# Performance work log

Measured on AMD Instinct MI355X. Metric: run time of the kernel, lower is better.

## Reference

```python
import jax, jax.numpy as jnp
import numpy as np

N_NODES = 50000
N_EDGES = 600000
BAG = 16
VOCAB = 10000
EMB = 128
HID = 128
N_CLASSES = 10
N_GRAPHS = 512
PAD_IDX = 1


def setup_inputs() -> dict:
    key = jax.random.key(0)
    ks = jax.random.split(key, 12)
    x_tokens = jax.random.randint(ks[0], (N_NODES, BAG), 0, VOCAB)
    src = jax.random.randint(ks[1], (N_EDGES,), 0, N_NODES)
    dst = jax.random.randint(ks[2], (N_EDGES,), 0, N_NODES)
    edge_index = jnp.stack([src, dst])
    batch = jnp.sort(jax.random.randint(ks[3], (N_NODES,), 0, N_GRAPHS))
    # rows 0,1 are zero in the original (weights[2:] filled from pretrained vectors)
    emb_table = (jax.random.normal(ks[4], (VOCAB, EMB)) * 0.02).at[:2].set(0.0)
    s = 1.0 / np.sqrt(EMB)
    w1_l = jax.random.normal(ks[5], (HID, EMB)) * s
    b1 = jnp.zeros((HID,), jnp.float32)
    w1_r = jax.random.normal(ks[6], (HID, EMB)) * s
    w2_l = jax.random.normal(ks[7], (HID, HID)) * s
    b2 = jnp.zeros((HID,), jnp.float32)
    w2_r = jax.random.normal(ks[8], (HID, HID)) * s
    w_out = jax.random.normal(ks[9], (N_CLASSES, HID)) * s
    b_out = jnp.zeros((N_CLASSES,), jnp.float32)
    return {"x_tokens": x_tokens, "edge_index": edge_index, "batch": batch,
            "emb_table": emb_table, "w1_l": w1_l, "b1": b1, "w1_r": w1_r,
            "w2_l": w2_l, "b2": b2, "w2_r": w2_r, "w_out": w_out, "b_out": b_out}


def _embedding_bag_mean(tokens, table):
    # nn.EmbeddingBag mode='mean' with padding_idx: padding tokens excluded from mean
    emb = table[tokens]                                  # [N, BAG, D]
    mask = (tokens != PAD_IDX)[..., None].astype(table.dtype)
    total = jnp.sum(emb * mask, axis=1)                  # [N, D]
    cnt = jnp.clip(jnp.sum(mask, axis=1), 1.0)           # [N, 1]
    return total / cnt


def _sage_conv(x, src, dst, w_l, b_l, w_r):
    # PyG SAGEConv: lin_l(mean_{j in N(i)} x_j) + lin_r(x_i); lin_r has no bias
    n = x.shape[0]
    msg_sum = jax.ops.segment_sum(x[src], dst, num_segments=n)           # [N, D]
    deg = jax.ops.segment_sum(jnp.ones((src.shape[0], 1), x.dtype), dst,
                              num_segments=n)                             # [N, 1]
    aggr = msg_sum / jnp.clip(deg, 1.0)
    return aggr @ w_l.T + b_l + x @ w_r.T


def reference(x_tokens, edge_index, batch, emb_table, w1_l, b1, w1_r,
              w2_l, b2, w2_r, w_out, b_out):
    src, dst = edge_index[0], edge_index[1]
    x = _embedding_bag_mean(x_tokens, emb_table)                 # [N, EMB]
    x = jax.nn.relu(_sage_conv(x, src, dst, w1_l, b1, w1_r))     # [N, HID]
    x = jax.nn.relu(_sage_conv(x, src, dst, w2_l, b2, w2_r))     # [N, HID]
    # global_mean_pool over graph ids
    g_sum = jax.ops.segment_sum(x, batch, num_segments=N_GRAPHS)
    g_cnt = jax.ops.segment_sum(jnp.ones((x.shape[0], 1), x.dtype), batch,
                                num_segments=N_GRAPHS)
    g = g_sum / jnp.clip(g_cnt, 1.0)                             # [G, HID]
    return g @ w_out.T + b_out                                   # [G, C]
```

## Files before the change

### kernel.cpp

```cpp
#include <hip/hip_runtime.h>
#include <hip/hip_bf16.h>

#define NN 50000
#define NE 600000
#define BAG 16
#define EMB 128
#define HID 128
#define NC 10
#define NG 512
#define PAD_IDX 1
#define VOCAB 10000
#define SLOTS 64
#define TPAIRS (VOCAB * EMB / 2)
#define WPAIRS (4 * HID * EMB / 2)
#define EMVB (NN / 16)
#define NCHUNK 293
#define SCB (NCHUNK * 8)
#define NRANGE (NN / 8)
#define NTILES ((NN + 127) / 128)

typedef __attribute__((ext_vector_type(8))) short v8s;
typedef __attribute__((ext_vector_type(4))) float v4f;

__device__ __forceinline__ float bflo(unsigned u) { return __uint_as_float(u << 16); }
__device__ __forceinline__ float bfhi(unsigned u) { return __uint_as_float(u & 0xffff0000u); }
__device__ __forceinline__ unsigned short f2bf(float f) {
    unsigned u = __float_as_uint(f);
    return (unsigned short)((u + 0x7fffu + ((u >> 16) & 1u)) >> 16);
}
__device__ __forceinline__ void acc8(float* a, v8s v) {
    unsigned* u = (unsigned*)&v;
#pragma unroll
    for (int j = 0; j < 4; j++) {
        a[2 * j] += bflo(u[j]);
        a[2 * j + 1] += bfhi(u[j]);
    }
}

__global__ void k_conv(const float* __restrict__ t, unsigned short* __restrict__ tb,
                       const float* __restrict__ w1l, const float* __restrict__ w1r,
                       const float* __restrict__ w2l, const float* __restrict__ w2r,
                       unsigned short* __restrict__ wbf, int* __restrict__ cnt,
                       float* __restrict__ gsum, float* __restrict__ gcnt) {
    int i = blockIdx.x * blockDim.x + threadIdx.x;
    if (i < NN) cnt[i] = 0;
    if (i < NG * HID) gsum[i] = 0.f;
    if (i < NG) gcnt[i] = 0.f;
    if (i < TPAIRS) {
        float2 v = *(const float2*)(t + (size_t)i * 2);
        unsigned lo = f2bf(v.x), hi = f2bf(v.y);
        *(unsigned*)(tb + (size_t)i * 2) = lo | (hi << 16);
    } else if (i < TPAIRS + WPAIRS) {
        int j = i - TPAIRS;
        int k = j * 2;
        int arr = k >> 14;
        int o = k & 16383;
        const float* w = (arr == 0) ? w1l : (arr == 1) ? w1r : (arr == 2) ? w2l : w2r;
        float2 v = *(const float2*)(w + o);
        unsigned lo = f2bf(v.x), hi = f2bf(v.y);
        *(unsigned*)(wbf + k) = lo | (hi << 16);
    }
}

__global__ __launch_bounds__(256) void k_scatem(const int* __restrict__ src,
                                                const int* __restrict__ dst,
                                                int* __restrict__ cnt,
                                                unsigned short* __restrict__ slots,
                                                const int* __restrict__ tokens,
                                                const unsigned short* __restrict__ table,
                                                unsigned short* __restrict__ x0) {
    int b = blockIdx.x;
    int tid = threadIdx.x;

    if (b < SCB) {
        int r = b & 7, c = b >> 3;
        int e0 = c * 2048 + tid * 8;
        if (e0 < NE) {
            int lo = r * NRANGE, hi = lo + NRANGE;
            int4 s0 = *((const int4*)(src + e0));
            int4 s1 = *((const int4*)(src + e0) + 1);
            int4 d0 = *((const int4*)(dst + e0));
            int4 d1 = *((const int4*)(dst + e0) + 1);
            int ss[8] = {s0.x, s0.y, s0.z, s0.w, s1.x, s1.y, s1.z, s1.w};
            int dd[8] = {d0.x, d0.y, d0.z, d0.w, d1.x, d1.y, d1.z, d1.w};
#pragma unroll
            for (int j = 0; j < 8; j++) {
                if (dd[j] >= lo && dd[j] < hi) {
                    int p = atomicAdd(&cnt[dd[j]], 1);
                    if (p < SLOTS)
                        slots[(size_t)dd[j] * SLOTS + p] = (unsigned short)ss[j];
                }
            }
        }
        return;
    }

    int sl = tid & 15;
    int node = (b - SCB) * 16 + (tid >> 4);
    const int* tp = tokens + node * BAG;
    int tk[16];
    *(int4*)(tk) = *(const int4*)(tp);
    *(int4*)(tk + 4) = *(const int4*)(tp + 4);
    *(int4*)(tk + 8) = *(const int4*)(tp + 8);
    *(int4*)(tk + 12) = *(const int4*)(tp + 12);
    int c = 0;
#pragma unroll
    for (int t = 0; t < BAG; t++) c += (tk[t] != PAD_IDX);
    float a[8];
#pragma unroll
    for (int j = 0; j < 8; j++) a[j] = 0.f;
#pragma unroll
    for (int h = 0; h < 2; h++) {
        v8s v[8];
#pragma unroll
        for (int t = 0; t < 8; t++)
            v[t] = *(const v8s*)(table + (size_t)tk[h * 8 + t] * EMB + sl * 8);
#pragma unroll
        for (int t = 0; t < 8; t++) acc8(a, v[t]);
    }
    float inv = 1.0f / (float)(c > 0 ? c : 1);
    uint4 o;
    o.x = f2bf(a[0] * inv) | ((unsigned)f2bf(a[1] * inv) << 16);
    o.y = f2bf(a[2] * inv) | ((unsigned)f2bf(a[3] * inv) << 16);
    o.z = f2bf(a[4] * inv) | ((unsigned)f2bf(a[5] * inv) << 16);
    o.w = f2bf(a[6] * inv) | ((unsigned)f2bf(a[7] * inv) << 16);
    *(uint4*)(x0 + (size_t)node * EMB + sl * 8) = o;
}

__global__ __launch_bounds__(256) void k_aggr(const unsigned short* __restrict__ x,
                                              const int* __restrict__ cnt,
                                              const unsigned short* __restrict__ slots,
                                              unsigned short* __restrict__ aggr) {
    int node = blockIdx.x * 4 + (threadIdx.x >> 6);
    int lane = threadIdx.x & 63;
    if (node >= NN) return;
    int deg = cnt[node];
    int m = deg > SLOTS ? SLOTS : deg;
    int g = lane >> 4, sl = lane & 15;
    float a[8];
#pragma unroll
    for (int j = 0; j < 8; j++) a[j] = 0.f;
    int idx_l = slots[(size_t)node * SLOTS + ((lane < m) ? lane : 0)];
    int i = 0;
    for (; i + 8 <= m; i += 8) {
        int t0 = __shfl(idx_l, i + g, 64);
        int t1 = __shfl(idx_l, i + 4 + g, 64);
        v8s v0 = *(const v8s*)(x + (size_t)t0 * HID + sl * 8);
        v8s v1 = *(const v8s*)(x + (size_t)t1 * HID + sl * 8);
        acc8(a, v0);
        acc8(a, v1);
    }
    for (; i + 4 <= m; i += 4) {
        int t0 = __shfl(idx_l, i + g, 64);
        v8s v0 = *(const v8s*)(x + (size_t)t0 * HID + sl * 8);
        acc8(a, v0);
    }
    int rem = m - i;
    if (rem > 0) {
        int t0 = __shfl(idx_l, (g < rem) ? i + g : i, 64);
        v8s v0 = *(const v8s*)(x + (size_t)t0 * HID + sl * 8);
        if (g < rem) acc8(a, v0);
    }
#pragma unroll
    for (int j = 0; j < 8; j++) {
        a[j] += __shfl_xor(a[j], 16, 64);
        a[j] += __shfl_xor(a[j], 32, 64);
    }
    float inv = 1.0f / (float)(deg > 0 ? deg : 1);
    if (g == 0) {
        uint4 o;
        o.x = f2bf(a[0] * inv) | ((unsigned)f2bf(a[1] * inv) << 16);
        o.y = f2bf(a[2] * inv) | ((unsigned)f2bf(a[3] * inv) << 16);
        o.z = f2bf(a[4] * inv) | ((unsigned)f2bf(a[5] * inv) << 16);
        o.w = f2bf(a[6] * inv) | ((unsigned)f2bf(a[7] * inv) << 16);
        *(uint4*)(aggr + (size_t)node * HID + sl * 8) = o;
    }
}

__device__ __forceinline__ void sage_kloop(int row0, const unsigned short* __restrict__ xa,
                                           const unsigned short* __restrict__ xr,
                                           const unsigned short* __restrict__ wl,
                                           const unsigned short* __restrict__ wr,
                                           unsigned short* As, unsigned short* Bs,
                                           v4f acc[2][8]) {
    int tid = threadIdx.x;
    int wave = tid >> 6, lane = tid & 63;
    int q = lane >> 4, l16 = lane & 15;
    for (int kc = 0; kc < 8; kc++) {
        const unsigned short* Ag = (kc < 4) ? xa : xr;
        const unsigned short* Bg = (kc < 4) ? wl : wr;
        int koff = (kc & 3) * 32;
#pragma unroll
        for (int it = 0; it < 2; it++) {
            int seg = tid + it * 256;
            int r = seg >> 2, sg = seg & 3;
            int gr = row0 + r;
            if (gr > NN - 1) gr = NN - 1;
            v8s a = *(const v8s*)(Ag + (size_t)gr * HID + koff + sg * 8);
            *(v8s*)(As + r * 32 + sg * 8) = a;
            v8s b = *(const v8s*)(Bg + (size_t)r * HID + koff + sg * 8);
            *(v8s*)(Bs + r * 32 + sg * 8) = b;
        }
        __syncthreads();
        v8s a0 = *(const v8s*)(As + (wave * 32 + l16) * 32 + q * 8);
        v8s a1 = *(const v8s*)(As + (wave * 32 + 16 + l16) * 32 + q * 8);
#pragma unroll
        for (int nt = 0; nt < 8; nt++) {
            v8s b = *(const v8s*)(Bs + (nt * 16 + l16) * 32 + q * 8);
            acc[0][nt] = __builtin_amdgcn_mfma_f32_16x16x32_bf16(a0, b, acc[0][nt], 0, 0, 0);
            acc[1][nt] = __builtin_amdgcn_mfma_f32_16x16x32_bf16(a1, b, acc[1][nt], 0, 0, 0);
        }
        __syncthreads();
    }
}

__global__ __launch_bounds__(256) void k_sage(const unsigned short* __restrict__ xa,
                                              const unsigned short* __restrict__ xr,
                                              const unsigned short* __restrict__ wl,
                                              const unsigned short* __restrict__ wr,
                                              const float* __restrict__ bias,
                                              unsigned short* __restrict__ out) {
    __shared__ unsigned short As[128 * 32];
    __shared__ unsigned short Bs[128 * 32];
    int row0 = blockIdx.x * 128;
    v4f acc[2][8];
#pragma unroll
    for (int m = 0; m < 2; m++)
#pragma unroll
        for (int n = 0; n < 8; n++) acc[m][n] = (v4f){0.f, 0.f, 0.f, 0.f};
    sage_kloop(row0, xa, xr, wl, wr, As, Bs, acc);
    int tid = threadIdx.x;
    int wave = tid >> 6, lane = tid & 63;
    int q = lane >> 4, l16 = lane & 15;
#pragma unroll
    for (int nt = 0; nt < 8; nt++) {
        int col = nt * 16 + l16;
        float bv = bias[col];
#pragma unroll
        for (int mt = 0; mt < 2; mt++) {
#pragma unroll
            for (int r = 0; r < 4; r++) {
                int row = row0 + wave * 32 + mt * 16 + q * 4 + r;
                if (row < NN) {
                    float v = acc[mt][nt][r] + bv;
                    v = v > 0.f ? v : 0.f;
                    out[(size_t)row * HID + col] = f2bf(v);
                }
            }
        }
    }
}

__global__ __launch_bounds__(256) void k_sagepool(const unsigned short* __restrict__ xa,
                                                  const unsigned short* __restrict__ xr,
                                                  const unsigned short* __restrict__ wl,
                                                  const unsigned short* __restrict__ wr,
                                                  const float* __restrict__ bias,
                                                  const int* __restrict__ batch,
                                                  float* __restrict__ gsum,
                                                  float* __restrict__ gcnt) {
    __shared__ unsigned short smem[128 * 128];
    unsigned short* As = smem;
    unsigned short* Bs = smem + 128 * 32;
    int row0 = blockIdx.x * 128;
    v4f acc[2][8];
#pragma unroll
    for (int m = 0; m < 2; m++)
#pragma unroll
        for (int n = 0; n < 8; n++) acc[m][n] = (v4f){0.f, 0.f, 0.f, 0.f};
    sage_kloop(row0, xa, xr, wl, wr, As, Bs, acc);
    int tid = threadIdx.x;
    int wave = tid >> 6, lane = tid & 63;
    int q = lane >> 4, l16 = lane & 15;
#pragma unroll
    for (int nt = 0; nt < 8; nt++) {
        int col = nt * 16 + l16;
        float bv = bias[col];
#pragma unroll
        for (int mt = 0; mt < 2; mt++) {
#pragma unroll
            for (int r = 0; r < 4; r++) {
                int rl = wave * 32 + mt * 16 + q * 4 + r;
                float v = acc[mt][nt][r] + bv;
                v = v > 0.f ? v : 0.f;
                smem[rl * 128 + col] = f2bf(v);
            }
        }
    }
    __syncthreads();
    if (tid < 128) {
        int col = tid;
        int end = NN - row0;
        if (end > 128) end = 128;
        int cur = batch[row0];
        float acc_p = 0.f;
        int c = 0;
        for (int i = 0; i < end; i++) {
            int b = batch[row0 + i];
            if (b != cur) {
                atomicAdd(&gsum[cur * HID + col], acc_p);
                if (col == 0) atomicAdd(&gcnt[cur], (float)c);
                acc_p = 0.f;
                c = 0;
                cur = b;
            }
            acc_p += __uint_as_float(((unsigned)smem[i * 128 + col]) << 16);
            c++;
        }
        atomicAdd(&gsum[cur * HID + col], acc_p);
        if (col == 0) atomicAdd(&gcnt[cur], (float)c);
    }
}

__global__ __launch_bounds__(128) void k_final(const float* __restrict__ gsum,
                                               const float* __restrict__ gcnt,
                                               const float* __restrict__ w_out,
                                               const float* __restrict__ b_out,
                                               float* __restrict__ out) {
    __shared__ float mean[HID];
    int g = blockIdx.x, tid = threadIdx.x;
    mean[tid] = gsum[g * HID + tid] / fmaxf(gcnt[g], 1.0f);
    __syncthreads();
    if (tid < NC) {
        float s = b_out[tid];
#pragma unroll 16
        for (int d = 0; d < HID; d++) s += mean[d] * w_out[tid * HID + d];
        out[g * NC + tid] = s;
    }
}

extern "C" void kernel_launch(void* const* d_in, const int* in_sizes, int n_in,
                              void* d_out, int out_size, void* d_ws, size_t ws_size,
                              hipStream_t stream) {
    const int* x_tokens = (const int*)d_in[0];
    const int* edge = (const int*)d_in[1];
    const int* batch = (const int*)d_in[2];
    const float* emb_table = (const float*)d_in[3];
    const float* w1l = (const float*)d_in[4];
    const float* b1 = (const float*)d_in[5];
    const float* w1r = (const float*)d_in[6];
    const float* w2l = (const float*)d_in[7];
    const float* b2 = (const float*)d_in[8];
    const float* w2r = (const float*)d_in[9];
    const float* w_out = (const float*)d_in[10];
    const float* b_out = (const float*)d_in[11];
    float* out = (float*)d_out;

    char* ws = (char*)d_ws;
    size_t off = 0;
    auto alloc = [&](size_t bytes) {
        void* p = ws + off;
        off += (bytes + 255) & ~(size_t)255;
        return p;
    };
    int* cnt = (int*)alloc(NN * 4);
    unsigned short* slots = (unsigned short*)alloc((size_t)NN * SLOTS * 2);
    unsigned short* wbf = (unsigned short*)alloc(4 * HID * EMB * 2);
    float* gsum = (float*)alloc(NG * HID * 4);
    float* gcnt = (float*)alloc(NG * 4);
    unsigned short* x0 = (unsigned short*)alloc((size_t)NN * EMB * 2);
    unsigned short* x1 = (unsigned short*)alloc((size_t)NN * HID * 2);
    unsigned short* aggrb = (unsigned short*)alloc((size_t)NN * HID * 2);
    unsigned short* table_bf = x1;

    const int* srcp = edge;
    const int* dstp = edge + NE;

    k_conv<<<(TPAIRS + WPAIRS + 255) / 256, 256, 0, stream>>>(
        emb_table, table_bf, w1l, w1r, w2l, w2r, wbf, cnt, gsum, gcnt);
    k_scatem<<<SCB + EMVB, 256, 0, stream>>>(srcp, dstp, cnt, slots, x_tokens,
                                             table_bf, x0);
    k_aggr<<<(NN + 3) / 4, 256, 0, stream>>>(x0, cnt, slots, aggrb);
    k_sage<<<NTILES, 256, 0, stream>>>(aggrb, x0, wbf, wbf + 16384, b1, x1);
    k_aggr<<<(NN + 3) / 4, 256, 0, stream>>>(x1, cnt, slots, aggrb);
    k_sagepool<<<NTILES, 256, 0, stream>>>(aggrb, x1, wbf + 32768, wbf + 49152, b2,
                                           batch, gsum, gcnt);
    k_final<<<NG, 128, 0, stream>>>(gsum, gcnt, w_out, b_out, out);
}
```

Measured before the change: 208.9 us.

## Build neighbor slots via LDS-binned queues and a per-range CSR kernel

Edge scattering no longer does one global atomic per edge into per-node counters. Each edge block first bins its edges by destination range (125 ranges of 400 nodes) in shared memory, then appends each bin to a per-range global queue with one atomic per bin. A new kernel builds each range's counts and slot lists in LDS and writes them out with coalesced stores. The aim is to cut global atomic traffic and scattered 2-byte writes. The cost is an extra launch, a queue buffer, and a large static LDS allocation in the fused scatter/embedding kernel, which may lower occupancy for the embedding blocks.

```diff
diff --git a/kernel.cpp b/kernel.cpp
--- a/kernel.cpp
+++ b/kernel.cpp
@@ -14,9 +14,10 @@
 #define TPAIRS (VOCAB * EMB / 2)
 #define WPAIRS (4 * HID * EMB / 2)
 #define EMVB (NN / 16)
-#define NCHUNK 293
-#define SCB (NCHUNK * 8)
-#define NRANGE (NN / 8)
+#define NCH1 293
+#define RANGES 125
+#define RNODES 400
+#define QCAP 6400
 #define NTILES ((NN + 127) / 128)
 
 typedef __attribute__((ext_vector_type(8))) short v8s;
@@ -40,10 +41,10 @@
 __global__ void k_conv(const float* __restrict__ t, unsigned short* __restrict__ tb,
                        const float* __restrict__ w1l, const float* __restrict__ w1r,
                        const float* __restrict__ w2l, const float* __restrict__ w2r,
-                       unsigned short* __restrict__ wbf, int* __restrict__ cnt,
+                       unsigned short* __restrict__ wbf, int* __restrict__ qtail,
                        float* __restrict__ gsum, float* __restrict__ gcnt) {
     int i = blockIdx.x * blockDim.x + threadIdx.x;
-    if (i < NN) cnt[i] = 0;
+    if (i < RANGES) qtail[i] = 0;
     if (i < NG * HID) gsum[i] = 0.f;
     if (i < NG) gcnt[i] = 0.f;
     if (i < TPAIRS) {
@@ -64,19 +65,21 @@
 
 __global__ __launch_bounds__(256) void k_scatem(const int* __restrict__ src,
                                                 const int* __restrict__ dst,
-                                                int* __restrict__ cnt,
-                                                unsigned short* __restrict__ slots,
+                                                int* __restrict__ qtail,
+                                                unsigned* __restrict__ queue,
                                                 const int* __restrict__ tokens,
                                                 const unsigned short* __restrict__ table,
                                                 unsigned short* __restrict__ x0) {
+    __shared__ int qcntL[RANGES];
+    __shared__ unsigned qbufL[RANGES * 64];
     int b = blockIdx.x;
     int tid = threadIdx.x;
 
-    if (b < SCB) {
-        int r = b & 7, c = b >> 3;
-        int e0 = c * 2048 + tid * 8;
+    if (b < NCH1) {
+        for (int i = tid; i < RANGES; i += 256) qcntL[i] = 0;
+        __syncthreads();
+        int e0 = b * 2048 + tid * 8;
         if (e0 < NE) {
-            int lo = r * NRANGE, hi = lo + NRANGE;
             int4 s0 = *((const int4*)(src + e0));
             int4 s1 = *((const int4*)(src + e0) + 1);
             int4 d0 = *((const int4*)(dst + e0));
@@ -85,18 +88,26 @@
             int dd[8] = {d0.x, d0.y, d0.z, d0.w, d1.x, d1.y, d1.z, d1.w};
 #pragma unroll
             for (int j = 0; j < 8; j++) {
-                if (dd[j] >= lo && dd[j] < hi) {
-                    int p = atomicAdd(&cnt[dd[j]], 1);
-                    if (p < SLOTS)
-                        slots[(size_t)dd[j] * SLOTS + p] = (unsigned short)ss[j];
-                }
+                int q = dd[j] / RNODES;
+                unsigned pk = ((unsigned)(dd[j] - q * RNODES) << 16) | (unsigned)ss[j];
+                int pos = atomicAdd(&qcntL[q], 1);
+                if (pos < 64) qbufL[q * 64 + pos] = pk;
             }
         }
+        __syncthreads();
+        if (tid < RANGES) {
+            int n = qcntL[tid];
+            if (n > 64) n = 64;
+            int base = atomicAdd(&qtail[tid], n);
+            if (base + n > QCAP) n = (QCAP - base > 0) ? QCAP - base : 0;
+            unsigned* qp = queue + (size_t)tid * QCAP + base;
+            for (int k = 0; k < n; k++) qp[k] = qbufL[tid * 64 + k];
+        }
         return;
     }
 
     int sl = tid & 15;
-    int node = (b - SCB) * 16 + (tid >> 4);
+    int node = (b - NCH1) * 16 + (tid >> 4);
     const int* tp = tokens + node * BAG;
     int tk[16];
     *(int4*)(tk) = *(const int4*)(tp);
@@ -125,6 +136,31 @@
     o.z = f2bf(a[4] * inv) | ((unsigned)f2bf(a[5] * inv) << 16);
     o.w = f2bf(a[6] * inv) | ((unsigned)f2bf(a[7] * inv) << 16);
     *(uint4*)(x0 + (size_t)node * EMB + sl * 8) = o;
+}
+
+__global__ __launch_bounds__(256) void k_csr(const int* __restrict__ qtail,
+                                             const unsigned* __restrict__ queue,
+                                             int* __restrict__ cnt,
+                                             unsigned short* __restrict__ slots) {
+    __shared__ int cntL[RNODES];
+    __shared__ __align__(16) unsigned short slotsL[RNODES * SLOTS];
+    int r = blockIdx.x, tid = threadIdx.x;
+    for (int i = tid; i < RNODES; i += 256) cntL[i] = 0;
+    __syncthreads();
+    int n = qtail[r];
+    if (n > QCAP) n = QCAP;
+    const unsigned* qp = queue + (size_t)r * QCAP;
+    for (int i = tid; i < n; i += 256) {
+        unsigned u = qp[i];
+        int dl = u >> 16;
+        int p = atomicAdd(&cntL[dl], 1);
+        if (p < SLOTS) slotsL[dl * SLOTS + p] = (unsigned short)(u & 0xffffu);
+    }
+    __syncthreads();
+    uint4* gs = (uint4*)(slots + (size_t)r * RNODES * SLOTS);
+    const uint4* ls = (const uint4*)slotsL;
+    for (int i = tid; i < RNODES * SLOTS / 8; i += 256) gs[i] = ls[i];
+    for (int i = tid; i < RNODES; i += 256) cnt[r * RNODES + i] = cntL[i];
 }
 
 __global__ __launch_bounds__(256) void k_aggr(const unsigned short* __restrict__ x,
@@ -361,15 +397,18 @@
     unsigned short* x0 = (unsigned short*)alloc((size_t)NN * EMB * 2);
     unsigned short* x1 = (unsigned short*)alloc((size_t)NN * HID * 2);
     unsigned short* aggrb = (unsigned short*)alloc((size_t)NN * HID * 2);
+    unsigned* queue = (unsigned*)alloc((size_t)RANGES * QCAP * 4);
+    int* qtail = (int*)alloc(RANGES * 4);
     unsigned short* table_bf = x1;
 
     const int* srcp = edge;
     const int* dstp = edge + NE;
 
     k_conv<<<(TPAIRS + WPAIRS + 255) / 256, 256, 0, stream>>>(
-        emb_table, table_bf, w1l, w1r, w2l, w2r, wbf, cnt, gsum, gcnt);
-    k_scatem<<<SCB + EMVB, 256, 0, stream>>>(srcp, dstp, cnt, slots, x_tokens,
-                                             table_bf, x0);
+        emb_table, table_bf, w1l, w1r, w2l, w2r, wbf, qtail, gsum, gcnt);
+    k_scatem<<<NCH1 + EMVB, 256, 0, stream>>>(srcp, dstp, qtail, queue, x_tokens,
+                                              table_bf, x0);
+    k_csr<<<RANGES, 256, 0, stream>>>(qtail, queue, cnt, slots);
     k_aggr<<<(NN + 3) / 4, 256, 0, stream>>>(x0, cnt, slots, aggrb);
     k_sage<<<NTILES, 256, 0, stream>>>(aggrb, x0, wbf, wbf + 16384, b1, x1);
     k_aggr<<<(NN + 3) / 4, 256, 0, stream>>>(x1, cnt, slots, aggrb);
```

New measurement: 197.8 us. 5.3% less time.
